# Optimization experiments

Measured on AMD Instinct MI355X. Metric: run time of the kernel, lower is better.

Reference implementation:

```python
import jax, jax.numpy as jnp
import numpy as np

NUM_HEADS = 4
EPS = 1e-5


def conv1(W, b, z):
    # Conv1d with kernel_size=1 == channel-wise linear: (B, Cin, L) -> (B, Cout, L)
    return jnp.einsum('oi,bil->bol', W, z) + b[None, :, None]


def setup_inputs() -> dict:
    key = jax.random.key(0)
    ks = jax.random.split(key, 16)
    B, D, N = 2, 256, 4096
    s = 0.05
    return {
        'x': jax.random.normal(ks[0], (B, D, N), jnp.float32),
        'source': jax.random.normal(ks[1], (B, D, N), jnp.float32),
        'Wq': jax.random.normal(ks[2], (D, D), jnp.float32) * s,
        'bq': jax.random.normal(ks[3], (D,), jnp.float32) * s,
        'Wk': jax.random.normal(ks[4], (D, D), jnp.float32) * s,
        'bk': jax.random.normal(ks[5], (D,), jnp.float32) * s,
        'Wv': jax.random.normal(ks[6], (D, D), jnp.float32) * s,
        'bv': jax.random.normal(ks[7], (D,), jnp.float32) * s,
        'Wm': jax.random.normal(ks[8], (D, D), jnp.float32) * s,
        'bm': jax.random.normal(ks[9], (D,), jnp.float32) * s,
        'W1': jax.random.normal(ks[10], (2 * D, 2 * D), jnp.float32) * s,
        'b1': jax.random.normal(ks[11], (2 * D,), jnp.float32) * s,
        'W2': jax.random.normal(ks[12], (D, 2 * D), jnp.float32) * s,
        'b2': jax.random.normal(ks[13], (D,), jnp.float32) * s,
    }


def reference(x, source, Wq, bq, Wk, bk, Wv, bv, Wm, bm, W1, b1, W2, b2):
    B, D, N = x.shape
    M = source.shape[2]
    H = NUM_HEADS
    dim = D // H  # per-head dim; torch reshape splits channels as (dim, heads)

    q = conv1(Wq, bq, x).reshape(B, dim, H, N)
    k = conv1(Wk, bk, source).reshape(B, dim, H, M)
    v = conv1(Wv, bv, source).reshape(B, dim, H, M)

    scores = jnp.einsum('bdhn,bdhm->bhnm', q, k) / (dim ** 0.5)
    prob = jax.nn.softmax(scores, axis=-1)
    attn = jnp.einsum('bhnm,bdhm->bdhn', prob, v).reshape(B, D, N)

    message = conv1(Wm, bm, attn)

    h = conv1(W1, b1, jnp.concatenate([x, message], axis=1))
    # InstanceNorm1d (affine=False, biased var over L)
    mu = jnp.mean(h, axis=2, keepdims=True)
    var = jnp.mean((h - mu) ** 2, axis=2, keepdims=True)
    h = jax.nn.relu((h - mu) / jnp.sqrt(var + EPS))
    return conv1(W2, b2, h)
```

## Files before the change

### kernel.cpp

```cpp
#include <hip/hip_runtime.h>
#include <cstdint>
#include <cstddef>


typedef __attribute__((ext_vector_type(8))) short short8;
typedef __attribute__((ext_vector_type(4))) float floatx4;

__device__ __forceinline__ unsigned short f2bf(float x) {
  union { float f; unsigned int u; } c; c.f = x;
  unsigned int r = c.u + 0x7FFFu + ((c.u >> 16) & 1u);
  return (unsigned short)(r >> 16);
}
__device__ __forceinline__ float bf2f(unsigned short u) {
  union { unsigned int i; float f; } c; c.i = ((unsigned int)u) << 16; return c.f;
}
__device__ __forceinline__ void gload16(const void* g, void* l) {
  __builtin_amdgcn_global_load_lds(
      (const __attribute__((address_space(1))) unsigned int*)g,
      (__attribute__((address_space(3))) unsigned int*)l, 16, 0, 0);
}

#define LOG2E_8 0.18033688011112042f

__global__ __launch_bounds__(256) void tx_all(
    const float* __restrict__ x, const float* __restrict__ src,
    unsigned short* __restrict__ xb, unsigned short* __restrict__ sb,
    int C, int N)
{
  __shared__ float tile[32][33];
  const int which = blockIdx.z >> 1, b = blockIdx.z & 1;
  const float* X = which ? src : x;
  unsigned short* Y = which ? sb : xb;
  const int n0 = blockIdx.x * 32, c0 = blockIdx.y * 32;
  const int tc = threadIdx.x & 31, tr = threadIdx.x >> 5;
  #pragma unroll
  for (int i = 0; i < 4; ++i)
    tile[tr + i * 8][tc] = X[((size_t)b * C + c0 + tr + i * 8) * N + n0 + tc];
  __syncthreads();
  #pragma unroll
  for (int i = 0; i < 4; ++i)
    Y[((size_t)b * N + n0 + tr + i * 8) * C + c0 + tc] = f2bf(tile[tc][tr + i * 8]);
}

__global__ __launch_bounds__(256) void wprep(
    const float* __restrict__ Wq, const float* __restrict__ Wk,
    const float* __restrict__ Wv, const float* __restrict__ Wm,
    const float* __restrict__ W1, const float* __restrict__ W2,
    const float* __restrict__ bq, const float* __restrict__ bk,
    const float* __restrict__ bv, const float* __restrict__ bm,
    const float* __restrict__ b1, const float* __restrict__ b2,
    unsigned short* __restrict__ wqkv, unsigned short* __restrict__ wm_,
    unsigned short* __restrict__ w1_, unsigned short* __restrict__ w2_,
    float* __restrict__ biasb)
{
  const int bid = blockIdx.x, t = threadIdx.x;
  if (bid < 768) {
    const int idx = bid * 256 + t;
    const int op = idx >> 8, ip = idx & 255;
    const int grp = op >> 8, oo = op & 255;
    const int o = 4 * (oo & 63) + (oo >> 6);
    const float* W = grp == 0 ? Wq : grp == 1 ? Wk : Wv;
    const float sc = grp == 0 ? LOG2E_8 : 1.f;
    wqkv[idx] = f2bf(W[(size_t)o * 256 + ip] * sc);
  } else if (bid < 1024) {
    const int idx = (bid - 768) * 256 + t;
    const int op = idx >> 8, ip = idx & 255;
    const int i2 = 4 * (ip & 63) + (ip >> 6);
    wm_[idx] = f2bf(Wm[(size_t)op * 256 + i2]);
  } else if (bid < 2048) {
    const int idx = (bid - 1024) * 256 + t;
    w1_[idx] = f2bf(W1[idx]);
  } else if (bid < 2560) {
    const int idx = (bid - 2048) * 256 + t;
    w2_[idx] = f2bf(W2[idx]);
  } else {
    const int z = (bid - 2560) * 256 + t;
    if (z < 256)       biasb[z] = bq[4 * (z & 63) + (z >> 6)] * LOG2E_8;
    else if (z < 512)  { const int y = z - 256; biasb[z] = bk[4 * (y & 63) + (y >> 6)]; }
    else if (z < 768)  { const int y = z - 512; biasb[z] = bv[4 * (y & 63) + (y >> 6)]; }
    else if (z < 1024) biasb[z] = bm[z - 768];
    else if (z < 1536) biasb[z] = b1[z - 1024];
    else if (z < 1792) biasb[z] = b2[z - 1536];
  }
}

__global__ __launch_bounds__(256) void gemm128(
    const unsigned short* __restrict__ Wb, const float* __restrict__ bias,
    const unsigned short* __restrict__ X0, const unsigned short* __restrict__ X1,
    void* __restrict__ O0, void* __restrict__ O1, void* __restrict__ O2,
    int Co, int Ci, int Ci0, int N, int variant)
{
  const int n0 = blockIdx.x * 128;
  const int o0 = blockIdx.y * 128;
  const int b  = blockIdx.z;
  const int t  = threadIdx.x;
  const int w = t >> 6, lane = t & 63, qd = lane >> 4, l = lane & 15;
  const int oh = (w >> 1) * 64, nh = (w & 1) * 64;

  __shared__ unsigned short Wl[128 * 64];
  __shared__ unsigned short Xl[128 * 64];

  floatx4 acc[4][4];
  #pragma unroll
  for (int i = 0; i < 4; ++i)
    #pragma unroll
    for (int j = 0; j < 4; ++j) acc[i][j] = (floatx4){0.f, 0.f, 0.f, 0.f};

  for (int k0 = 0; k0 < Ci; k0 += 64) {
    const unsigned short* Xs; int cb, rl;
    if (variant == 1) { Xs = (o0 < 256) ? X0 : X1; cb = k0; rl = Ci; }
    else if (k0 < Ci0) { Xs = X0; cb = k0; rl = Ci0; }
    else               { Xs = X1; cb = k0 - Ci0; rl = Ci - Ci0; }
    __syncthreads();
    #pragma unroll
    for (int i = 0; i < 4; ++i) {
      const int idx = i * 256 + t;
      const int row = idx >> 3, pg = idx & 7, sg = pg ^ (row & 7);
      gload16(&Wb[(size_t)(o0 + row) * Ci + k0 + sg * 8], &Wl[row * 64 + pg * 8]);
      gload16(&Xs[((size_t)b * N + n0 + row) * rl + cb + sg * 8], &Xl[row * 64 + pg * 8]);
    }
    __syncthreads();

    short8 af[4][2], bf[4][2];
    #pragma unroll
    for (int i = 0; i < 4; ++i) {
      const int ar = oh + 16 * i + l;
      af[i][0] = *(const short8*)&Wl[ar * 64 + ((qd ^ (ar & 7))) * 8];
      af[i][1] = *(const short8*)&Wl[ar * 64 + (((4 + qd) ^ (ar & 7))) * 8];
    }
    #pragma unroll
    for (int j = 0; j < 4; ++j) {
      const int br = nh + 16 * j + l;
      bf[j][0] = *(const short8*)&Xl[br * 64 + ((qd ^ (br & 7))) * 8];
      bf[j][1] = *(const short8*)&Xl[br * 64 + (((4 + qd) ^ (br & 7))) * 8];
    }
    #pragma unroll
    for (int i = 0; i < 4; ++i)
      #pragma unroll
      for (int j = 0; j < 4; ++j) {
        acc[i][j] = __builtin_amdgcn_mfma_f32_16x16x32_bf16(af[i][0], bf[j][0], acc[i][j], 0, 0, 0);
        acc[i][j] = __builtin_amdgcn_mfma_f32_16x16x32_bf16(af[i][1], bf[j][1], acc[i][j], 0, 0, 0);
      }
  }

  const int osec = o0 + oh;
  #pragma unroll
  for (int i = 0; i < 4; ++i) {
    const int o4 = o0 + oh + 16 * i + qd * 4;
    const float4 bi = *(const float4*)&bias[o4];
    #pragma unroll
    for (int j = 0; j < 4; ++j) {
      const int n = n0 + nh + 16 * j + l;
      if (variant == 0) {
        unsigned short* C = (unsigned short*)O0;
        ushort4 pk;
        pk.x = f2bf(acc[i][j][0] + bi.x); pk.y = f2bf(acc[i][j][1] + bi.y);
        pk.z = f2bf(acc[i][j][2] + bi.z); pk.w = f2bf(acc[i][j][3] + bi.w);
        *(ushort4*)&C[((size_t)b * N + n) * Co + o4] = pk;
      } else if (variant == 1) {
        if (osec < 256) {
          unsigned short* C = (unsigned short*)O0;
          ushort4 pk;
          pk.x = f2bf(acc[i][j][0] + bi.x); pk.y = f2bf(acc[i][j][1] + bi.y);
          pk.z = f2bf(acc[i][j][2] + bi.z); pk.w = f2bf(acc[i][j][3] + bi.w);
          *(ushort4*)&C[((size_t)b * N + n) * 256 + o4] = pk;
        } else if (osec < 512) {
          unsigned short* C = (unsigned short*)O1;
          ushort4 pk;
          pk.x = f2bf(acc[i][j][0] + bi.x); pk.y = f2bf(acc[i][j][1] + bi.y);
          pk.z = f2bf(acc[i][j][2] + bi.z); pk.w = f2bf(acc[i][j][3] + bi.w);
          *(ushort4*)&C[((size_t)b * N + n) * 256 + (o4 - 256)] = pk;
        } else {
          unsigned short* C = (unsigned short*)O2;
          #pragma unroll
          for (int rg = 0; rg < 4; ++rg) {
            const int op = o4 - 512 + rg, h = op >> 6, d = op & 63;
            C[(((size_t)b * 4 + h) * 64 + d) * N + n] =
                f2bf(acc[i][j][rg] + ((const float*)&bi)[rg]);
          }
        }
      } else {
        float* C = (float*)O0;
        #pragma unroll
        for (int rg = 0; rg < 4; ++rg)
          C[((size_t)b * Co + o4 + rg) * N + n] = acc[i][j][rg] + ((const float*)&bi)[rg];
      }
    }
  }
}

__global__ __launch_bounds__(256) void attn_mfma(
    const unsigned short* __restrict__ qb, const unsigned short* __restrict__ kb,
    const unsigned short* __restrict__ vh, unsigned short* __restrict__ Opart,
    float* __restrict__ liPart, int N)
{
  const int qt = blockIdx.x;
  const int h  = blockIdx.y;
  const int b  = blockIdx.z >> 2, s = blockIdx.z & 3;
  const int n0 = qt * 128;
  const int t  = threadIdx.x;
  const int w = t >> 6, lane = t & 63, qd = lane >> 4, l = lane & 15;

  __shared__ unsigned short Kl[64 * 64];
  __shared__ unsigned short Vl[64 * 64];
  __shared__ unsigned short Pl[4][16 * 64];

  const unsigned short* qp0 = &qb[((size_t)b * N + n0 + 16 * w + l) * 256 + h * 64];
  const unsigned short* qp1 = qp0 + (size_t)64 * 256;
  short8 aQ[2][2];
  aQ[0][0] = *(const short8*)&qp0[qd * 8];
  aQ[0][1] = *(const short8*)&qp0[32 + qd * 8];
  aQ[1][0] = *(const short8*)&qp1[qd * 8];
  aQ[1][1] = *(const short8*)&qp1[32 + qd * 8];

  floatx4 accO[2][4];
  #pragma unroll
  for (int qs = 0; qs < 2; ++qs)
    #pragma unroll
    for (int ds = 0; ds < 4; ++ds) accO[qs][ds] = (floatx4){0.f, 0.f, 0.f, 0.f};
  float li[2][4] = {};

  const int j0base = s * 1024;
  for (int jt = 0; jt < 16; ++jt) {
    const int j0 = j0base + jt * 64;
    __syncthreads();
    #pragma unroll
    for (int i = 0; i < 2; ++i) {
      const int idx = i * 256 + t;
      const int row = idx >> 3, pg = idx & 7, sg = pg ^ (row & 7);
      gload16(&kb[((size_t)b * N + j0 + row) * 256 + h * 64 + sg * 8],
              &Kl[row * 64 + pg * 8]);
      gload16(&vh[(((size_t)b * 4 + h) * 64 + row) * N + j0 + sg * 8],
              &Vl[row * 64 + pg * 8]);
    }
    __syncthreads();

    short8 kf[4][2], vf[4][2];
    #pragma unroll
    for (int js = 0; js < 4; ++js) {
      const int br = 16 * js + l;
      kf[js][0] = *(const short8*)&Kl[br * 64 + ((qd ^ (br & 7))) * 8];
      kf[js][1] = *(const short8*)&Kl[br * 64 + (((4 + qd) ^ (br & 7))) * 8];
      vf[js][0] = *(const short8*)&Vl[br * 64 + ((qd ^ (br & 7))) * 8];
      vf[js][1] = *(const short8*)&Vl[br * 64 + (((4 + qd) ^ (br & 7))) * 8];
    }

    #pragma unroll
    for (int qs = 0; qs < 2; ++qs) {
      floatx4 S[4];
      #pragma unroll
      for (int js = 0; js < 4; ++js) {
        floatx4 a = (floatx4){0.f, 0.f, 0.f, 0.f};
        a = __builtin_amdgcn_mfma_f32_16x16x32_bf16(aQ[qs][0], kf[js][0], a, 0, 0, 0);
        a = __builtin_amdgcn_mfma_f32_16x16x32_bf16(aQ[qs][1], kf[js][1], a, 0, 0, 0);
        S[js] = a;
      }
      #pragma unroll
      for (int js = 0; js < 4; ++js) {
        const int kg = 2 * js + (l >> 3);
        #pragma unroll
        for (int rg = 0; rg < 4; ++rg) {
          const float p = __builtin_exp2f(S[js][rg]);
          li[qs][rg] += p;
          union { float f; unsigned int u; } cv; cv.f = p;
          const int qr = qd * 4 + rg;
          Pl[w][qr * 64 + ((kg ^ (qr & 7))) * 8 + (l & 7)] =
              (unsigned short)((cv.u + 0x8000u) >> 16);
        }
      }
      const short8 aP0 = *(const short8*)&Pl[w][l * 64 + ((qd ^ (l & 7))) * 8];
      const short8 aP1 = *(const short8*)&Pl[w][l * 64 + (((4 + qd) ^ (l & 7))) * 8];
      #pragma unroll
      for (int ds = 0; ds < 4; ++ds) {
        accO[qs][ds] = __builtin_amdgcn_mfma_f32_16x16x32_bf16(aP0, vf[ds][0], accO[qs][ds], 0, 0, 0);
        accO[qs][ds] = __builtin_amdgcn_mfma_f32_16x16x32_bf16(aP1, vf[ds][1], accO[qs][ds], 0, 0, 0);
      }
    }
  }

  const size_t obase = ((((size_t)b * 4 + h) * 4 + s) * 32 + qt) * 128;
  #pragma unroll
  for (int qs = 0; qs < 2; ++qs)
    #pragma unroll
    for (int rg = 0; rg < 4; ++rg) {
      float sum = li[qs][rg];
      sum += __shfl_xor(sum, 1);
      sum += __shfl_xor(sum, 2);
      sum += __shfl_xor(sum, 4);
      sum += __shfl_xor(sum, 8);
      const int q = qs * 64 + 16 * w + qd * 4 + rg;
      #pragma unroll
      for (int ds = 0; ds < 4; ++ds)
        Opart[(obase + q) * 64 + 16 * ds + l] = f2bf(accO[qs][ds][rg]);
      if (l == 0) liPart[obase + q] = sum;
    }
}

__global__ __launch_bounds__(256) void attn_combine(
    const unsigned short* __restrict__ Opart, const float* __restrict__ liPart,
    unsigned short* __restrict__ atb, int N)
{
  const int qt = blockIdx.x, h = blockIdx.y, b = blockIdx.z;
  const int t = threadIdx.x;
  const int q = t >> 1, d0 = (t & 1) * 32;

  float li = 0.f;
  size_t idx[4];
  #pragma unroll
  for (int s = 0; s < 4; ++s) {
    idx[s] = ((((size_t)b * 4 + h) * 4 + s) * 32 + qt) * 128 + q;
    li += liPart[idx[s]];
  }
  const float inv = 1.f / li;

  float o[32];
  #pragma unroll
  for (int c = 0; c < 32; ++c) o[c] = 0.f;
  #pragma unroll
  for (int s = 0; s < 4; ++s) {
    #pragma unroll
    for (int c4 = 0; c4 < 4; ++c4) {
      const short8 v = *(const short8*)&Opart[idx[s] * 64 + d0 + c4 * 8];
      #pragma unroll
      for (int j = 0; j < 8; ++j) o[c4 * 8 + j] += bf2f((unsigned short)v[j]);
    }
  }
  unsigned short* dst = &atb[((size_t)b * N + qt * 128 + q) * 256 + h * 64 + d0];
  #pragma unroll
  for (int c4 = 0; c4 < 4; ++c4) {
    ushort4 pk;
    pk.x = f2bf(o[c4 * 8 + 0] * inv); pk.y = f2bf(o[c4 * 8 + 1] * inv);
    pk.z = f2bf(o[c4 * 8 + 2] * inv); pk.w = f2bf(o[c4 * 8 + 3] * inv);
    *(ushort4*)&dst[c4 * 8] = pk;
    pk.x = f2bf(o[c4 * 8 + 4] * inv); pk.y = f2bf(o[c4 * 8 + 5] * inv);
    pk.z = f2bf(o[c4 * 8 + 6] * inv); pk.w = f2bf(o[c4 * 8 + 7] * inv);
    *(ushort4*)&dst[c4 * 8 + 4] = pk;
  }
}

__global__ __launch_bounds__(256) void in_stats(
    const unsigned short* __restrict__ H, float* __restrict__ Ps,
    float* __restrict__ Ps2, int N)
{
  const int cg = blockIdx.x, ns = blockIdx.y, b = blockIdx.z, t = threadIdx.x;
  const int c0 = cg * 64 + (t & 7) * 8;
  float s[8] = {}, s2[8] = {};
  #pragma unroll
  for (int i = 0; i < 8; ++i) {
    const int n = ns * 256 + (t >> 3) + i * 32;
    const short8 hv = *(const short8*)&H[((size_t)b * N + n) * 512 + c0];
    #pragma unroll
    for (int j = 0; j < 8; ++j) {
      const float f = bf2f((unsigned short)hv[j]);
      s[j] += f; s2[j] += f * f;
    }
  }
  __shared__ float rs[32][64], rs2[32][64];
  #pragma unroll
  for (int j = 0; j < 8; ++j) {
    rs[t >> 3][(t & 7) * 8 + j] = s[j];
    rs2[t >> 3][(t & 7) * 8 + j] = s2[j];
  }
  __syncthreads();
  if (t < 64) {
    float a = 0.f, a2 = 0.f;
    #pragma unroll
    for (int r = 0; r < 32; ++r) { a += rs[r][t]; a2 += rs2[r][t]; }
    const size_t o = ((size_t)ns * 2 + b) * 512 + cg * 64 + t;
    Ps[o] = a; Ps2[o] = a2;
  }
}

__global__ __launch_bounds__(256) void in_norm(
    unsigned short* __restrict__ H, const float* __restrict__ Ps,
    const float* __restrict__ Ps2, int N)
{
  const int cg = blockIdx.x, ns = blockIdx.y, b = blockIdx.z, t = threadIdx.x;
  __shared__ float muS[64], ivS[64];
  if (t < 64) {
    const int c = cg * 64 + t;
    float s = 0.f, s2 = 0.f;
    for (int k = 0; k < 16; ++k) {
      s  += Ps [((size_t)k * 2 + b) * 512 + c];
      s2 += Ps2[((size_t)k * 2 + b) * 512 + c];
    }
    const float mu = s / (float)N;
    const float var = fmaxf(s2 / (float)N - mu * mu, 0.f);
    muS[t] = mu;
    ivS[t] = rsqrtf(var + 1e-5f);
  }
  __syncthreads();
  const int c0 = cg * 64 + (t & 7) * 8;
  float mu[8], iv[8];
  #pragma unroll
  for (int j = 0; j < 8; ++j) {
    mu[j] = muS[(t & 7) * 8 + j];
    iv[j] = ivS[(t & 7) * 8 + j];
  }
  #pragma unroll
  for (int i = 0; i < 8; ++i) {
    const int n = ns * 256 + (t >> 3) + i * 32;
    unsigned short* p = &H[((size_t)b * N + n) * 512 + c0];
    short8 hv = *(const short8*)p;
    #pragma unroll
    for (int j = 0; j < 8; ++j) {
      const float f = fmaxf((bf2f((unsigned short)hv[j]) - mu[j]) * iv[j], 0.f);
      hv[j] = (short)f2bf(f);
    }
    *(short8*)p = hv;
  }
}

extern "C" void kernel_launch(void* const* d_in, const int* in_sizes, int n_in,
                              void* d_out, int out_size, void* d_ws, size_t ws_size,
                              hipStream_t stream)
{
  const int B = 2, D = 256, N = 4096;

  const float* x   = (const float*)d_in[0];
  const float* src = (const float*)d_in[1];
  const float* Wq  = (const float*)d_in[2];  const float* bq = (const float*)d_in[3];
  const float* Wk  = (const float*)d_in[4];  const float* bk = (const float*)d_in[5];
  const float* Wv  = (const float*)d_in[6];  const float* bv = (const float*)d_in[7];
  const float* Wm  = (const float*)d_in[8];  const float* bm = (const float*)d_in[9];
  const float* W1  = (const float*)d_in[10]; const float* b1 = (const float*)d_in[11];
  const float* W2  = (const float*)d_in[12]; const float* b2 = (const float*)d_in[13];
  float* out = (float*)d_out;

  char* ws = (char*)d_ws;
  const size_t MB = 1u << 20;
  unsigned short* xb  = (unsigned short*)(ws + 0 * MB);
  unsigned short* sb  = (unsigned short*)(ws + 4 * MB);
  unsigned short* qbf = (unsigned short*)(ws + 8 * MB);
  unsigned short* kbf = (unsigned short*)(ws + 12 * MB);
  unsigned short* vhb = (unsigned short*)(ws + 16 * MB);
  unsigned short* atb = (unsigned short*)(ws + 20 * MB);
  unsigned short* Opart = (unsigned short*)(ws + 24 * MB);
  unsigned short* msb = (unsigned short*)(ws + 24 * MB);
  unsigned short* hb  = (unsigned short*)(ws + 28 * MB);
  float* liPart = (float*)(ws + 41 * MB);
  unsigned short* wqkvb = (unsigned short*)(ws + 42 * MB);
  unsigned short* wmb = wqkvb + 768 * 256;
  unsigned short* w1b = wmb + 256 * 256;
  unsigned short* w2b = w1b + 512 * 512;
  float* biasb = (float*)(ws + 44 * MB);
  float* Ps    = biasb + 2048;
  float* Ps2   = Ps + 16 * 2 * 512;

  const dim3 blk(256);

  tx_all<<<dim3(N / 32, D / 32, 2 * B), blk, 0, stream>>>(x, src, xb, sb, D, N);
  wprep<<<dim3(2567), blk, 0, stream>>>(Wq, Wk, Wv, Wm, W1, W2,
                                        bq, bk, bv, bm, b1, b2,
                                        wqkvb, wmb, w1b, w2b, biasb);

  gemm128<<<dim3(N / 128, 6, B), blk, 0, stream>>>(
      wqkvb, biasb, xb, sb, qbf, kbf, vhb, 768, 256, 256, N, 1);

  attn_mfma<<<dim3(N / 128, 4, B * 4), blk, 0, stream>>>(
      qbf, kbf, vhb, Opart, liPart, N);
  attn_combine<<<dim3(N / 128, 4, B), blk, 0, stream>>>(Opart, liPart, atb, N);

  gemm128<<<dim3(N / 128, 2, B), blk, 0, stream>>>(
      wmb, biasb + 768, atb, atb, msb, nullptr, nullptr, 256, 256, 256, N, 0);

  gemm128<<<dim3(N / 128, 4, B), blk, 0, stream>>>(
      w1b, biasb + 1024, xb, msb, hb, nullptr, nullptr, 512, 512, 256, N, 0);

  in_stats<<<dim3(8, 16, B), blk, 0, stream>>>(hb, Ps, Ps2, N);
  in_norm<<<dim3(8, 16, B), blk, 0, stream>>>(hb, Ps, Ps2, N);

  gemm128<<<dim3(N / 128, 2, B), blk, 0, stream>>>(
      w2b, biasb + 1536, hb, hb, out, nullptr, nullptr, 256, 512, 512, N, 2);
}
```

Measured before the change: 233.5 us.

## Fuse instance-norm statistics into W1 GEMM epilogue; double K/V tile in attention

The W1 GEMM epilogue now reduces per-channel sum and sum-of-squares across lanes with shuffles and accumulates them into global buffers with atomics. This removes the separate in_stats kernel and its re-read of H, and the accumulators are zeroed by an extra block in wprep. Separately, the attention kernel loads 128 keys per iteration into two LDS panels, which halves the number of barrier pairs. The cost is atomic contention and extra LDS use, and the statistics are now taken from fp32 values before bf16 rounding.

```diff
diff --git a/kernel.cpp b/kernel.cpp
--- a/kernel.cpp
+++ b/kernel.cpp
@@ -49,9 +49,9 @@
     const float* __restrict__ bq, const float* __restrict__ bk,
     const float* __restrict__ bv, const float* __restrict__ bm,
     const float* __restrict__ b1, const float* __restrict__ b2,
-    unsigned short* __restrict__ wqkv, unsigned short* __restrict__ wm_,
-    unsigned short* __restrict__ w1_, unsigned short* __restrict__ w2_,
-    float* __restrict__ biasb)
+    unsigned short* __restrict__ wqkv, unsigned short* __restrict__ wmb,
+    unsigned short* __restrict__ w1b, unsigned short* __restrict__ w2b,
+    float* __restrict__ biasb, float* __restrict__ Pzero)
 {
   const int bid = blockIdx.x, t = threadIdx.x;
   if (bid < 768) {
@@ -64,16 +64,16 @@
     wqkv[idx] = f2bf(W[(size_t)o * 256 + ip] * sc);
   } else if (bid < 1024) {
     const int idx = (bid - 768) * 256 + t;
-    const int op = idx >> 8, ip = idx & 255;
+    const int o = idx >> 8, ip = idx & 255;
     const int i2 = 4 * (ip & 63) + (ip >> 6);
-    wm_[idx] = f2bf(Wm[(size_t)op * 256 + i2]);
+    wmb[idx] = f2bf(Wm[(size_t)o * 256 + i2]);
   } else if (bid < 2048) {
     const int idx = (bid - 1024) * 256 + t;
-    w1_[idx] = f2bf(W1[idx]);
+    w1b[idx] = f2bf(W1[idx]);
   } else if (bid < 2560) {
     const int idx = (bid - 2048) * 256 + t;
-    w2_[idx] = f2bf(W2[idx]);
-  } else {
+    w2b[idx] = f2bf(W2[idx]);
+  } else if (bid < 2567) {
     const int z = (bid - 2560) * 256 + t;
     if (z < 256)       biasb[z] = bq[4 * (z & 63) + (z >> 6)] * LOG2E_8;
     else if (z < 512)  { const int y = z - 256; biasb[z] = bk[4 * (y & 63) + (y >> 6)]; }
@@ -81,6 +81,9 @@
     else if (z < 1024) biasb[z] = bm[z - 768];
     else if (z < 1536) biasb[z] = b1[z - 1024];
     else if (z < 1792) biasb[z] = b2[z - 1536];
+  } else {
+    #pragma unroll
+    for (int k = 0; k < 8; ++k) Pzero[k * 256 + t] = 0.f;
   }
 }
 
@@ -88,7 +91,8 @@
     const unsigned short* __restrict__ Wb, const float* __restrict__ bias,
     const unsigned short* __restrict__ X0, const unsigned short* __restrict__ X1,
     void* __restrict__ O0, void* __restrict__ O1, void* __restrict__ O2,
-    int Co, int Ci, int Ci0, int N, int variant)
+    int Co, int Ci, int Ci0, int N, int variant,
+    float* __restrict__ Ps, float* __restrict__ Ps2)
 {
   const int n0 = blockIdx.x * 128;
   const int o0 = blockIdx.y * 128;
@@ -144,6 +148,49 @@
   }
 
   const int osec = o0 + oh;
+  if (variant == 4) {
+    unsigned short* C = (unsigned short*)O0;
+    float s1[4][4], s2[4][4];
+    #pragma unroll
+    for (int i = 0; i < 4; ++i) {
+      const int o4 = o0 + oh + 16 * i + qd * 4;
+      const float4 bi = *(const float4*)&bias[o4];
+      #pragma unroll
+      for (int rg = 0; rg < 4; ++rg) { s1[i][rg] = 0.f; s2[i][rg] = 0.f; }
+      #pragma unroll
+      for (int j = 0; j < 4; ++j) {
+        const int n = n0 + nh + 16 * j + l;
+        float v[4];
+        v[0] = acc[i][j][0] + bi.x; v[1] = acc[i][j][1] + bi.y;
+        v[2] = acc[i][j][2] + bi.z; v[3] = acc[i][j][3] + bi.w;
+        ushort4 pk;
+        pk.x = f2bf(v[0]); pk.y = f2bf(v[1]); pk.z = f2bf(v[2]); pk.w = f2bf(v[3]);
+        *(ushort4*)&C[((size_t)b * N + n) * Co + o4] = pk;
+        #pragma unroll
+        for (int rg = 0; rg < 4; ++rg) {
+          s1[i][rg] += v[rg];
+          s2[i][rg] += v[rg] * v[rg];
+        }
+      }
+    }
+    #pragma unroll
+    for (int i = 0; i < 4; ++i)
+      #pragma unroll
+      for (int rg = 0; rg < 4; ++rg) {
+        float a = s1[i][rg], c2 = s2[i][rg];
+        a  += __shfl_xor(a, 1);  c2 += __shfl_xor(c2, 1);
+        a  += __shfl_xor(a, 2);  c2 += __shfl_xor(c2, 2);
+        a  += __shfl_xor(a, 4);  c2 += __shfl_xor(c2, 4);
+        a  += __shfl_xor(a, 8);  c2 += __shfl_xor(c2, 8);
+        if (l == 0) {
+          const int o = o0 + oh + 16 * i + qd * 4 + rg;
+          atomicAdd(&Ps [b * 512 + o], a);
+          atomicAdd(&Ps2[b * 512 + o], c2);
+        }
+      }
+    return;
+  }
+
   #pragma unroll
   for (int i = 0; i < 4; ++i) {
     const int o4 = o0 + oh + 16 * i + qd * 4;
@@ -201,8 +248,8 @@
   const int t  = threadIdx.x;
   const int w = t >> 6, lane = t & 63, qd = lane >> 4, l = lane & 15;
 
-  __shared__ unsigned short Kl[64 * 64];
-  __shared__ unsigned short Vl[64 * 64];
+  __shared__ unsigned short Kl[2][64 * 64];
+  __shared__ unsigned short Vl[2][64 * 64];
   __shared__ unsigned short Pl[4][16 * 64];
 
   const unsigned short* qp0 = &qb[((size_t)b * N + n0 + 16 * w + l) * 256 + h * 64];
@@ -221,59 +268,67 @@
   float li[2][4] = {};
 
   const int j0base = s * 1024;
-  for (int jt = 0; jt < 16; ++jt) {
-    const int j0 = j0base + jt * 64;
+  for (int jt = 0; jt < 8; ++jt) {
+    const int j0 = j0base + jt * 128;
     __syncthreads();
     #pragma unroll
-    for (int i = 0; i < 2; ++i) {
+    for (int i = 0; i < 4; ++i) {
       const int idx = i * 256 + t;
-      const int row = idx >> 3, pg = idx & 7, sg = pg ^ (row & 7);
-      gload16(&kb[((size_t)b * N + j0 + row) * 256 + h * 64 + sg * 8],
-              &Kl[row * 64 + pg * 8]);
-      gload16(&vh[(((size_t)b * 4 + h) * 64 + row) * N + j0 + sg * 8],
-              &Vl[row * 64 + pg * 8]);
+      {
+        const int row = idx >> 3, pg = idx & 7, sg = pg ^ (row & 7);
+        gload16(&kb[((size_t)b * N + j0 + row) * 256 + h * 64 + sg * 8],
+                &Kl[row >> 6][(row & 63) * 64 + pg * 8]);
+      }
+      {
+        const int pan = idx >> 9, d = (idx >> 3) & 63, pg = idx & 7;
+        const int sg = pg ^ (d & 7);
+        gload16(&vh[(((size_t)b * 4 + h) * 64 + d) * N + j0 + pan * 64 + sg * 8],
+                &Vl[pan][d * 64 + pg * 8]);
+      }
     }
     __syncthreads();
 
-    short8 kf[4][2], vf[4][2];
-    #pragma unroll
-    for (int js = 0; js < 4; ++js) {
-      const int br = 16 * js + l;
-      kf[js][0] = *(const short8*)&Kl[br * 64 + ((qd ^ (br & 7))) * 8];
-      kf[js][1] = *(const short8*)&Kl[br * 64 + (((4 + qd) ^ (br & 7))) * 8];
-      vf[js][0] = *(const short8*)&Vl[br * 64 + ((qd ^ (br & 7))) * 8];
-      vf[js][1] = *(const short8*)&Vl[br * 64 + (((4 + qd) ^ (br & 7))) * 8];
-    }
-
-    #pragma unroll
-    for (int qs = 0; qs < 2; ++qs) {
-      floatx4 S[4];
+    #pragma unroll
+    for (int p = 0; p < 2; ++p) {
+      short8 kf[4][2], vf[4][2];
       #pragma unroll
       for (int js = 0; js < 4; ++js) {
-        floatx4 a = (floatx4){0.f, 0.f, 0.f, 0.f};
-        a = __builtin_amdgcn_mfma_f32_16x16x32_bf16(aQ[qs][0], kf[js][0], a, 0, 0, 0);
-        a = __builtin_amdgcn_mfma_f32_16x16x32_bf16(aQ[qs][1], kf[js][1], a, 0, 0, 0);
-        S[js] = a;
-      }
-      #pragma unroll
-      for (int js = 0; js < 4; ++js) {
-        const int kg = 2 * js + (l >> 3);
+        const int br = 16 * js + l;
+        kf[js][0] = *(const short8*)&Kl[p][br * 64 + ((qd ^ (br & 7))) * 8];
+        kf[js][1] = *(const short8*)&Kl[p][br * 64 + (((4 + qd) ^ (br & 7))) * 8];
+        vf[js][0] = *(const short8*)&Vl[p][br * 64 + ((qd ^ (br & 7))) * 8];
+        vf[js][1] = *(const short8*)&Vl[p][br * 64 + (((4 + qd) ^ (br & 7))) * 8];
+      }
+      #pragma unroll
+      for (int qs = 0; qs < 2; ++qs) {
+        floatx4 S[4];
         #pragma unroll
-        for (int rg = 0; rg < 4; ++rg) {
-          const float p = __builtin_exp2f(S[js][rg]);
-          li[qs][rg] += p;
-          union { float f; unsigned int u; } cv; cv.f = p;
-          const int qr = qd * 4 + rg;
-          Pl[w][qr * 64 + ((kg ^ (qr & 7))) * 8 + (l & 7)] =
-              (unsigned short)((cv.u + 0x8000u) >> 16);
-        }
-      }
-      const short8 aP0 = *(const short8*)&Pl[w][l * 64 + ((qd ^ (l & 7))) * 8];
-      const short8 aP1 = *(const short8*)&Pl[w][l * 64 + (((4 + qd) ^ (l & 7))) * 8];
-      #pragma unroll
-      for (int ds = 0; ds < 4; ++ds) {
-        accO[qs][ds] = __builtin_amdgcn_mfma_f32_16x16x32_bf16(aP0, vf[ds][0], accO[qs][ds], 0, 0, 0);
-        accO[qs][ds] = __builtin_amdgcn_mfma_f32_16x16x32_bf16(aP1, vf[ds][1], accO[qs][ds], 0, 0, 0);
+        for (int js = 0; js < 4; ++js) {
+          floatx4 a = (floatx4){0.f, 0.f, 0.f, 0.f};
+          a = __builtin_amdgcn_mfma_f32_16x16x32_bf16(aQ[qs][0], kf[js][0], a, 0, 0, 0);
+          a = __builtin_amdgcn_mfma_f32_16x16x32_bf16(aQ[qs][1], kf[js][1], a, 0, 0, 0);
+          S[js] = a;
+        }
+        #pragma unroll
+        for (int js = 0; js < 4; ++js) {
+          const int kg = 2 * js + (l >> 3);
+          #pragma unroll
+          for (int rg = 0; rg < 4; ++rg) {
+            const float pv = __builtin_exp2f(S[js][rg]);
+            li[qs][rg] += pv;
+            union { float f; unsigned int u; } cv; cv.f = pv;
+            const int qr = qd * 4 + rg;
+            Pl[w][qr * 64 + ((kg ^ (qr & 7))) * 8 + (l & 7)] =
+                (unsigned short)((cv.u + 0x8000u) >> 16);
+          }
+        }
+        const short8 aP0 = *(const short8*)&Pl[w][l * 64 + ((qd ^ (l & 7))) * 8];
+        const short8 aP1 = *(const short8*)&Pl[w][l * 64 + (((4 + qd) ^ (l & 7))) * 8];
+        #pragma unroll
+        for (int ds = 0; ds < 4; ++ds) {
+          accO[qs][ds] = __builtin_amdgcn_mfma_f32_16x16x32_bf16(aP0, vf[ds][0], accO[qs][ds], 0, 0, 0);
+          accO[qs][ds] = __builtin_amdgcn_mfma_f32_16x16x32_bf16(aP1, vf[ds][1], accO[qs][ds], 0, 0, 0);
+        }
       }
     }
   }
@@ -338,39 +393,6 @@
   }
 }
 
-__global__ __launch_bounds__(256) void in_stats(
-    const unsigned short* __restrict__ H, float* __restrict__ Ps,
-    float* __restrict__ Ps2, int N)
-{
-  const int cg = blockIdx.x, ns = blockIdx.y, b = blockIdx.z, t = threadIdx.x;
-  const int c0 = cg * 64 + (t & 7) * 8;
-  float s[8] = {}, s2[8] = {};
-  #pragma unroll
-  for (int i = 0; i < 8; ++i) {
-    const int n = ns * 256 + (t >> 3) + i * 32;
-    const short8 hv = *(const short8*)&H[((size_t)b * N + n) * 512 + c0];
-    #pragma unroll
-    for (int j = 0; j < 8; ++j) {
-      const float f = bf2f((unsigned short)hv[j]);
-      s[j] += f; s2[j] += f * f;
-    }
-  }
-  __shared__ float rs[32][64], rs2[32][64];
-  #pragma unroll
-  for (int j = 0; j < 8; ++j) {
-    rs[t >> 3][(t & 7) * 8 + j] = s[j];
-    rs2[t >> 3][(t & 7) * 8 + j] = s2[j];
-  }
-  __syncthreads();
-  if (t < 64) {
-    float a = 0.f, a2 = 0.f;
-    #pragma unroll
-    for (int r = 0; r < 32; ++r) { a += rs[r][t]; a2 += rs2[r][t]; }
-    const size_t o = ((size_t)ns * 2 + b) * 512 + cg * 64 + t;
-    Ps[o] = a; Ps2[o] = a2;
-  }
-}
-
 __global__ __launch_bounds__(256) void in_norm(
     unsigned short* __restrict__ H, const float* __restrict__ Ps,
     const float* __restrict__ Ps2, int N)
@@ -379,13 +401,8 @@
   __shared__ float muS[64], ivS[64];
   if (t < 64) {
     const int c = cg * 64 + t;
-    float s = 0.f, s2 = 0.f;
-    for (int k = 0; k < 16; ++k) {
-      s  += Ps [((size_t)k * 2 + b) * 512 + c];
-      s2 += Ps2[((size_t)k * 2 + b) * 512 + c];
-    }
-    const float mu = s / (float)N;
-    const float var = fmaxf(s2 / (float)N - mu * mu, 0.f);
+    const float mu = Ps[b * 512 + c] / (float)N;
+    const float var = fmaxf(Ps2[b * 512 + c] / (float)N - mu * mu, 0.f);
     muS[t] = mu;
     ivS[t] = rsqrtf(var + 1e-5f);
   }
@@ -445,31 +462,33 @@
   unsigned short* w2b = w1b + 512 * 512;
   float* biasb = (float*)(ws + 44 * MB);
   float* Ps    = biasb + 2048;
-  float* Ps2   = Ps + 16 * 2 * 512;
+  float* Ps2   = Ps + 1024;
 
   const dim3 blk(256);
 
   tx_all<<<dim3(N / 32, D / 32, 2 * B), blk, 0, stream>>>(x, src, xb, sb, D, N);
-  wprep<<<dim3(2567), blk, 0, stream>>>(Wq, Wk, Wv, Wm, W1, W2,
+  wprep<<<dim3(2568), blk, 0, stream>>>(Wq, Wk, Wv, Wm, W1, W2,
                                         bq, bk, bv, bm, b1, b2,
-                                        wqkvb, wmb, w1b, w2b, biasb);
+                                        wqkvb, wmb, w1b, w2b, biasb, Ps);
 
   gemm128<<<dim3(N / 128, 6, B), blk, 0, stream>>>(
-      wqkvb, biasb, xb, sb, qbf, kbf, vhb, 768, 256, 256, N, 1);
+      wqkvb, biasb, xb, sb, qbf, kbf, vhb, 768, 256, 256, N, 1, nullptr, nullptr);
 
   attn_mfma<<<dim3(N / 128, 4, B * 4), blk, 0, stream>>>(
       qbf, kbf, vhb, Opart, liPart, N);
   attn_combine<<<dim3(N / 128, 4, B), blk, 0, stream>>>(Opart, liPart, atb, N);
 
   gemm128<<<dim3(N / 128, 2, B), blk, 0, stream>>>(
-      wmb, biasb + 768, atb, atb, msb, nullptr, nullptr, 256, 256, 256, N, 0);
+      wmb, biasb + 768, atb, atb, msb, nullptr, nullptr, 256, 256, 256, N, 0,
+      nullptr, nullptr);
 
   gemm128<<<dim3(N / 128, 4, B), blk, 0, stream>>>(
-      w1b, biasb + 1024, xb, msb, hb, nullptr, nullptr, 512, 512, 256, N, 0);
-
-  in_stats<<<dim3(8, 16, B), blk, 0, stream>>>(hb, Ps, Ps2, N);
+      w1b, biasb + 1024, xb, msb, hb, nullptr, nullptr,
+      512, 512, 256, N, 4, Ps, Ps2);
+
   in_norm<<<dim3(8, 16, B), blk, 0, stream>>>(hb, Ps, Ps2, N);
 
   gemm128<<<dim3(N / 128, 2, B), blk, 0, stream>>>(
-      w2b, biasb + 1536, hb, hb, out, nullptr, nullptr, 256, 512, 512, N, 2);
-}
+      w2b, biasb + 1536, hb, hb, out, nullptr, nullptr,
+      256, 512, 512, N, 2, nullptr, nullptr);
+}
```

Result: slower. 261.1 us (+11.8%).
